# Kernel tuning notes

Measured on AMD Instinct MI355X. Metric: run time of the kernel, lower is better.

## Reference

```python
import jax, jax.numpy as jnp
import numpy as np

D_MODEL = 1024
NUM_HEADS = 16
HEAD_DIM = D_MODEL // NUM_HEADS
SEQ_LEN = 2048
BATCH = 2
THETA = 10000.0


def apply_rope(x, token_positions):
    # x: (..., seq, head_dim); token_positions: (seq,)
    d_k = x.shape[-1]
    inv_freq = 1.0 / (THETA ** (jnp.arange(0, d_k, 2, dtype=jnp.float32) / d_k))  # (d_k/2,)
    angle = token_positions.astype(jnp.float32)[:, None] * inv_freq[None, :]       # (seq, d_k/2)
    cos, sin = jnp.cos(angle), jnp.sin(angle)
    xr = x.reshape(*x.shape[:-1], d_k // 2, 2)
    a, b = xr[..., 0], xr[..., 1]  # real, imag parts of consecutive pairs
    # complex multiply (a + ib) * (cos + i sin)
    out_r = a * cos - b * sin
    out_i = a * sin + b * cos
    return jnp.stack([out_r, out_i], axis=-1).reshape(x.shape)


def setup_inputs() -> dict:
    key = jax.random.key(0)
    ks = jax.random.split(key, 5)
    std = np.sqrt(2.0 / (D_MODEL + D_MODEL))
    return {
        "x": jax.random.normal(ks[0], (BATCH, SEQ_LEN, D_MODEL), dtype=jnp.float32),
        "Wq": jax.random.normal(ks[1], (D_MODEL, D_MODEL), dtype=jnp.float32) * std,
        "Wk": jax.random.normal(ks[2], (D_MODEL, D_MODEL), dtype=jnp.float32) * std,
        "Wv": jax.random.normal(ks[3], (D_MODEL, D_MODEL), dtype=jnp.float32) * std,
        "Wo": jax.random.normal(ks[4], (D_MODEL, D_MODEL), dtype=jnp.float32) * std,
        "token_positions": jnp.arange(SEQ_LEN, dtype=jnp.int32),
    }


def reference(x, Wq, Wk, Wv, Wo, token_positions):
    B, L, D = x.shape
    H, Dh = NUM_HEADS, HEAD_DIM

    def proj(W):  # '... d_in, d_out d_in -> ... d_out' then split heads -> (B,H,L,Dh)
        y = jnp.einsum('bld,ed->ble', x, W)
        return y.reshape(B, L, H, Dh).transpose(0, 2, 1, 3)

    q = apply_rope(proj(Wq), token_positions)
    k = apply_rope(proj(Wk), token_positions)
    v = proj(Wv)

    scores = jnp.einsum('bhqd,bhkd->bhqk', q, k) / jnp.sqrt(jnp.float32(Dh))  # (B,H,L,L)
    causal = jnp.tril(jnp.ones((L, L), dtype=bool))
    scores = jnp.where(causal, scores, -jnp.inf)
    attn = jax.nn.softmax(scores, axis=-1)
    o = jnp.einsum('bhqk,bhkd->bhqd', attn, v)  # (B,H,L,Dh)
    o = o.transpose(0, 2, 1, 3).reshape(B, L, D)
    return jnp.einsum('bld,ed->ble', o, Wo)
```

## Files before the change

kernel.cpp:

```cpp
#include <hip/hip_runtime.h>

typedef __bf16 bf16;
typedef __attribute__((ext_vector_type(8))) __bf16 bf16x8;
typedef __attribute__((ext_vector_type(4))) __bf16 bf16x4;
typedef __attribute__((ext_vector_type(4))) float f32x4;

__device__ inline bf16 f2bf(float f) {
  unsigned u = __builtin_bit_cast(unsigned, f);
  u += 0x7fff + ((u >> 16) & 1);
  unsigned short h = (unsigned short)(u >> 16);
  return __builtin_bit_cast(bf16, h);
}

__device__ inline void gl_lds16(const bf16* g, bf16* l) {
  __builtin_amdgcn_global_load_lds(
      (const __attribute__((address_space(1))) void*)g,
      (__attribute__((address_space(3))) void*)l, 16, 0, 0);
}

__global__ __launch_bounds__(256) void cvt_kernel(
    const float* __restrict__ x, const float* __restrict__ wq,
    const float* __restrict__ wk, const float* __restrict__ wv,
    const float* __restrict__ wo, bf16* __restrict__ dst) {
  int idx = (blockIdx.x * 256 + threadIdx.x) * 4;
  const float* src;
  if (idx < 4194304) {
    src = x + idx;
  } else {
    int j = idx - 4194304;
    int w = j >> 20;
    const float* sw = (w == 0) ? wq : (w == 1) ? wk : (w == 2) ? wv : wo;
    src = sw + (j & 1048575);
  }
  float4 f = *(const float4*)src;
  bf16x4 o = {f2bf(f.x), f2bf(f.y), f2bf(f.z), f2bf(f.w)};
  *(bf16x4*)(dst + idx) = o;
}

__global__ __launch_bounds__(256) void rope_tab_kernel(
    const int* __restrict__ pos, float* __restrict__ tab) {
  int gid = blockIdx.x * 256 + threadIdx.x;
  int tok = gid >> 5, j = gid & 31;
  float freq = exp2f(-(float)(2 * j) * 0.20762051f);
  float angle = (float)pos[tok] * freq;
  float sn, cs;
  sincosf(angle, &sn, &cs);
  *(float2*)(tab + tok * 64 + j * 2) = make_float2(cs, sn);
}

__global__ __launch_bounds__(256) void gemm_qkv_kernel(
    const bf16* __restrict__ xb, const bf16* __restrict__ wb,
    const float* __restrict__ tab,
    bf16* __restrict__ Qb, bf16* __restrict__ Kb, bf16* __restrict__ Vtb) {
  __shared__ __align__(16) bf16 As[128 * 32];
  __shared__ __align__(16) bf16 Bs[128 * 32];
  int tid = threadIdx.x;
  int lane = tid & 63, w = tid >> 6;
  int l15 = lane & 15, quad = lane >> 4;
  int mb = blockIdx.y * 128, nb = blockIdx.x * 128;
  int mq = (w & 1) * 64, nq = (w >> 1) * 64;
  const bf16* agp = xb + (size_t)(mb + w * 16 + (lane >> 2)) * 1024 + (lane & 3) * 8;
  const bf16* bgp = wb + (size_t)(nb + w * 16 + (lane >> 2)) * 1024 + (lane & 3) * 8;
  bf16* alp = As + (w * 16) * 32;
  bf16* blp = Bs + (w * 16) * 32;
  f32x4 acc[4][4];
#pragma unroll
  for (int i = 0; i < 4; ++i)
#pragma unroll
    for (int j = 0; j < 4; ++j)
      for (int r = 0; r < 4; ++r) acc[i][j][r] = 0.f;
  for (int kt = 0; kt < 32; ++kt) {
    gl_lds16(agp, alp);
    gl_lds16(agp + 65536, alp + 2048);
    gl_lds16(bgp, blp);
    gl_lds16(bgp + 65536, blp + 2048);
    agp += 32; bgp += 32;
    __syncthreads();
    bf16x8 af[4], bfr[4];
#pragma unroll
    for (int mt = 0; mt < 4; ++mt)
      af[mt] = *(const bf16x8*)(As + (mq + mt * 16 + l15) * 32 + quad * 8);
#pragma unroll
    for (int nt = 0; nt < 4; ++nt)
      bfr[nt] = *(const bf16x8*)(Bs + (nq + nt * 16 + l15) * 32 + quad * 8);
#pragma unroll
    for (int mt = 0; mt < 4; ++mt)
#pragma unroll
      for (int nt = 0; nt < 4; ++nt)
        acc[mt][nt] = __builtin_amdgcn_mfma_f32_16x16x32_bf16(af[mt], bfr[nt], acc[mt][nt], 0, 0, 0);
    __syncthreads();
  }
#pragma unroll
  for (int nt = 0; nt < 4; ++nt) {
    int e = nb + nq + nt * 16 + l15;
    bool isv = (e >= 2048);
    int d = e & 63;
    int h = (e & 1023) >> 6;
    int tbase = d & ~1;
#pragma unroll
    for (int mt = 0; mt < 4; ++mt) {
#pragma unroll
      for (int r = 0; r < 4; ++r) {
        int m = mb + mq + mt * 16 + quad * 4 + r;
        int b = m >> 11, ltok = m & 2047;
        float val = acc[mt][nt][r];
        float p = __shfl_xor(val, 1);
        float outv;
        if (!isv) {
          float2 cs2 = *(const float2*)(tab + ltok * 64 + tbase);
          outv = (e & 1) ? (p * cs2.y + val * cs2.x) : (val * cs2.x - p * cs2.y);
        } else {
          outv = val;
        }
        bf16 bv = f2bf(outv);
        if (e < 1024) {
          Qb[(((b << 4) + h) * 2048 + ltok) * 64 + d] = bv;
        } else if (!isv) {
          Kb[(((b << 4) + h) * 2048 + ltok) * 64 + d] = bv;
        } else {
          Vtb[(((b << 4) + h) * 64 + d) * 2048 + ltok] = bv;
        }
      }
    }
  }
}

#define SCALE_L2E 0.18033688f
__global__ __launch_bounds__(256) void attn_kernel(
    const bf16* __restrict__ Qb, const bf16* __restrict__ Kb,
    const bf16* __restrict__ Vtb, bf16* __restrict__ Ob) {
  __shared__ __align__(16) bf16 Ks[64 * 64];
  __shared__ __align__(16) bf16 Vs[64 * 64];
  __shared__ __align__(16) bf16 pbuf[4][16 * 72];
  int tid = threadIdx.x;
  int lane = tid & 63, w = tid >> 6;
  int l15 = lane & 15, quad = lane >> 4;
  int bidx = blockIdx.x;
  int bh = bidx & 31;
  int qt = 31 - (bidx >> 5);
  int qbase = qt * 64;
  const bf16* Qp = Qb + (size_t)bh * 131072;
  const bf16* Kp = Kb + (size_t)bh * 131072;
  const bf16* Vp = Vtb + (size_t)bh * 131072;
  int r8 = lane >> 3;
  int gsw8 = (lane & 7) ^ r8;
  int g0 = quad ^ (l15 & 7);
  int g1 = (4 + quad) ^ (l15 & 7);
  bf16x8 qf[2];
#pragma unroll
  for (int c = 0; c < 2; ++c)
    qf[c] = *(const bf16x8*)(Qp + (size_t)(qbase + w * 16 + l15) * 64 + c * 32 + quad * 8);
  f32x4 oacc[4];
#pragma unroll
  for (int dt = 0; dt < 4; ++dt)
    for (int r = 0; r < 4; ++r) oacc[dt][r] = 0.f;
  float lpart = 0.f;
  int qmin_w = qbase + w * 16;
  int qmax_w = qmin_w + 15;
  int ntiles = qt + 1;

  for (int t = 0; t < ntiles; ++t) {
    int kb = t * 64;
    {
      const bf16* ksrc = Kp + (size_t)(kb + w * 16 + r8) * 64 + gsw8 * 8;
      bf16* kdst = &Ks[(w * 16) * 64];
      gl_lds16(ksrc, kdst);
      gl_lds16(ksrc + 8 * 64, kdst + 8 * 64);
      const bf16* vsrc = Vp + (size_t)(w * 16 + r8) * 2048 + kb + gsw8 * 8;
      bf16* vdst = &Vs[(w * 16) * 64];
      gl_lds16(vsrc, vdst);
      gl_lds16(vsrc + 8 * 2048, vdst + 8 * 64);
    }
    __syncthreads();
    if (kb <= qmax_w) {
      bf16x8 kf[4][2], vf[4][2];
#pragma unroll
      for (int kt = 0; kt < 4; ++kt) {
        kf[kt][0] = *(const bf16x8*)(&Ks[(kt * 16 + l15) * 64 + g0 * 8]);
        kf[kt][1] = *(const bf16x8*)(&Ks[(kt * 16 + l15) * 64 + g1 * 8]);
      }
#pragma unroll
      for (int dt = 0; dt < 4; ++dt) {
        vf[dt][0] = *(const bf16x8*)(&Vs[(dt * 16 + l15) * 64 + g0 * 8]);
        vf[dt][1] = *(const bf16x8*)(&Vs[(dt * 16 + l15) * 64 + g1 * 8]);
      }
      int q = qmin_w + l15;
      f32x4 s[4];
#pragma unroll
      for (int kt = 0; kt < 4; ++kt) {
        for (int r = 0; r < 4; ++r) s[kt][r] = 0.f;
        s[kt] = __builtin_amdgcn_mfma_f32_16x16x32_bf16(kf[kt][0], qf[0], s[kt], 0, 0, 0);
        s[kt] = __builtin_amdgcn_mfma_f32_16x16x32_bf16(kf[kt][1], qf[1], s[kt], 0, 0, 0);
      }
      float pe[16];
      if (kb + 63 > qmin_w) {
#pragma unroll
        for (int kt = 0; kt < 4; ++kt)
#pragma unroll
          for (int r = 0; r < 4; ++r) {
            int key = kb + kt * 16 + quad * 4 + r;
            pe[kt * 4 + r] = (key <= q) ? exp2f(s[kt][r] * SCALE_L2E) : 0.f;
          }
      } else {
#pragma unroll
        for (int kt = 0; kt < 4; ++kt)
#pragma unroll
          for (int r = 0; r < 4; ++r) pe[kt * 4 + r] = exp2f(s[kt][r] * SCALE_L2E);
      }
#pragma unroll
      for (int i = 0; i < 16; ++i) lpart += pe[i];
#pragma unroll
      for (int kt = 0; kt < 4; ++kt) {
        bf16x4 pw = {f2bf(pe[kt * 4]), f2bf(pe[kt * 4 + 1]), f2bf(pe[kt * 4 + 2]), f2bf(pe[kt * 4 + 3])};
        *(bf16x4*)&pbuf[w][l15 * 72 + kt * 16 + quad * 4] = pw;
      }
      bf16x8 pb0 = *(const bf16x8*)&pbuf[w][l15 * 72 + quad * 8];
      bf16x8 pb1 = *(const bf16x8*)&pbuf[w][l15 * 72 + 32 + quad * 8];
#pragma unroll
      for (int dt = 0; dt < 4; ++dt) {
        oacc[dt] = __builtin_amdgcn_mfma_f32_16x16x32_bf16(vf[dt][0], pb0, oacc[dt], 0, 0, 0);
        oacc[dt] = __builtin_amdgcn_mfma_f32_16x16x32_bf16(vf[dt][1], pb1, oacc[dt], 0, 0, 0);
      }
    }
    __syncthreads();
  }
  float lrun = lpart;
  lrun += __shfl_xor(lrun, 16);
  lrun += __shfl_xor(lrun, 32);
  int b0 = bh >> 4, h = bh & 15;
  float inv = 1.f / lrun;
  int q = qmin_w + l15;
  bf16* obase = Ob + ((size_t)(b0 * 2048 + q)) * 1024 + h * 64;
#pragma unroll
  for (int dt = 0; dt < 4; ++dt)
#pragma unroll
    for (int r = 0; r < 4; ++r)
      obase[dt * 16 + quad * 4 + r] = f2bf(oacc[dt][r] * inv);
}

__global__ __launch_bounds__(256) void gemm_out_kernel(
    const bf16* __restrict__ Ob, const bf16* __restrict__ wob,
    float* __restrict__ out) {
  __shared__ __align__(16) bf16 As[64 * 32];
  __shared__ __align__(16) bf16 Bs[64 * 32];
  int tid = threadIdx.x;
  int lane = tid & 63, w = tid >> 6;
  int l15 = lane & 15, quad = lane >> 4;
  int mb = blockIdx.y * 64, nb = blockIdx.x * 64;
  int mq = (w & 1) * 32, nq = (w >> 1) * 32;
  const bf16* agp = Ob + (size_t)(mb + w * 16 + (lane >> 2)) * 1024 + (lane & 3) * 8;
  const bf16* bgp = wob + (size_t)(nb + w * 16 + (lane >> 2)) * 1024 + (lane & 3) * 8;
  bf16* alp = As + (w * 16) * 32;
  bf16* blp = Bs + (w * 16) * 32;
  f32x4 acc[2][2];
#pragma unroll
  for (int i = 0; i < 2; ++i)
#pragma unroll
    for (int j = 0; j < 2; ++j)
      for (int r = 0; r < 4; ++r) acc[i][j][r] = 0.f;
  for (int kt = 0; kt < 32; ++kt) {
    gl_lds16(agp, alp);
    gl_lds16(bgp, blp);
    agp += 32; bgp += 32;
    __syncthreads();
    bf16x8 af[2], bfr[2];
#pragma unroll
    for (int mt = 0; mt < 2; ++mt)
      af[mt] = *(const bf16x8*)(As + (mq + mt * 16 + l15) * 32 + quad * 8);
#pragma unroll
    for (int nt = 0; nt < 2; ++nt)
      bfr[nt] = *(const bf16x8*)(Bs + (nq + nt * 16 + l15) * 32 + quad * 8);
#pragma unroll
    for (int mt = 0; mt < 2; ++mt)
#pragma unroll
      for (int nt = 0; nt < 2; ++nt)
        acc[mt][nt] = __builtin_amdgcn_mfma_f32_16x16x32_bf16(af[mt], bfr[nt], acc[mt][nt], 0, 0, 0);
    __syncthreads();
  }
#pragma unroll
  for (int mt = 0; mt < 2; ++mt)
#pragma unroll
    for (int nt = 0; nt < 2; ++nt)
#pragma unroll
      for (int r = 0; r < 4; ++r)
        out[(size_t)(mb + mq + mt * 16 + quad * 4 + r) * 1024 + nb + nq + nt * 16 + l15] = acc[mt][nt][r];
}

extern "C" void kernel_launch(void* const* d_in, const int* in_sizes, int n_in,
                              void* d_out, int out_size, void* d_ws, size_t ws_size,
                              hipStream_t stream) {
  const float* x  = (const float*)d_in[0];
  const float* wq = (const float*)d_in[1];
  const float* wk = (const float*)d_in[2];
  const float* wv = (const float*)d_in[3];
  const float* wo = (const float*)d_in[4];
  const int* pos  = (const int*)d_in[5];
  float* out = (float*)d_out;
  bf16* wsb = (bf16*)d_ws;
  bf16* xb  = wsb;
  bf16* wb  = wsb + 4194304;
  bf16* Qb  = wsb + 8388608;
  bf16* Kb  = wsb + 12582912;
  bf16* Vtb = wsb + 16777216;
  bf16* Obf = wsb + 20971520;
  float* tab = (float*)Obf;
  hipLaunchKernelGGL(cvt_kernel, dim3(8192), dim3(256), 0, stream, x, wq, wk, wv, wo, wsb);
  hipLaunchKernelGGL(rope_tab_kernel, dim3(256), dim3(256), 0, stream, pos, tab);
  hipLaunchKernelGGL(gemm_qkv_kernel, dim3(24, 32), dim3(256), 0, stream, xb, wb, tab, Qb, Kb, Vtb);
  hipLaunchKernelGGL(attn_kernel, dim3(1024), dim3(256), 0, stream, Qb, Kb, Vtb, Obf);
  hipLaunchKernelGGL(gemm_out_kernel, dim3(16, 64), dim3(256), 0, stream, Obf, wb + 3 * 1048576, out);
}
```

Measured before the change: 227.5 us.

## Restructure QKV GEMM with K=64 swizzled LDS tiles, block remap, and coalesced V stores

Merges the RoPE table computation into the conversion kernel to drop one launch. The QKV GEMM now loads K-tiles of 64 with an XOR-swizzled LDS layout to cut bank conflicts and halve the barrier count. It also remaps the 1D grid so neighbouring blocks share operands in cache. The V epilogue transposes through LDS so V^T is written with 16-byte coalesced stores instead of scattered 2-byte writes. In exchange it doubles LDS use per block and adds extra barriers in the V path.

```diff
diff --git a/kernel.cpp b/kernel.cpp
--- a/kernel.cpp
+++ b/kernel.cpp
@@ -21,7 +21,18 @@
 __global__ __launch_bounds__(256) void cvt_kernel(
     const float* __restrict__ x, const float* __restrict__ wq,
     const float* __restrict__ wk, const float* __restrict__ wv,
-    const float* __restrict__ wo, bf16* __restrict__ dst) {
+    const float* __restrict__ wo, bf16* __restrict__ dst,
+    const int* __restrict__ pos, float* __restrict__ tab) {
+  if (blockIdx.x >= 8192) {
+    int gid = (blockIdx.x - 8192) * 256 + threadIdx.x;
+    int tok = gid >> 5, j = gid & 31;
+    float freq = exp2f(-(float)(2 * j) * 0.20762051f);
+    float angle = (float)pos[tok] * freq;
+    float sn, cs;
+    sincosf(angle, &sn, &cs);
+    *(float2*)(tab + tok * 64 + j * 2) = make_float2(cs, sn);
+    return;
+  }
   int idx = (blockIdx.x * 256 + threadIdx.x) * 4;
   const float* src;
   if (idx < 4194304) {
@@ -37,90 +48,103 @@
   *(bf16x4*)(dst + idx) = o;
 }
 
-__global__ __launch_bounds__(256) void rope_tab_kernel(
-    const int* __restrict__ pos, float* __restrict__ tab) {
-  int gid = blockIdx.x * 256 + threadIdx.x;
-  int tok = gid >> 5, j = gid & 31;
-  float freq = exp2f(-(float)(2 * j) * 0.20762051f);
-  float angle = (float)pos[tok] * freq;
-  float sn, cs;
-  sincosf(angle, &sn, &cs);
-  *(float2*)(tab + tok * 64 + j * 2) = make_float2(cs, sn);
-}
-
 __global__ __launch_bounds__(256) void gemm_qkv_kernel(
     const bf16* __restrict__ xb, const bf16* __restrict__ wb,
     const float* __restrict__ tab,
     bf16* __restrict__ Qb, bf16* __restrict__ Kb, bf16* __restrict__ Vtb) {
-  __shared__ __align__(16) bf16 As[128 * 32];
-  __shared__ __align__(16) bf16 Bs[128 * 32];
+  __shared__ __align__(16) bf16 smem[16384];
+  bf16* As = smem;
+  bf16* Bs = smem + 8192;
   int tid = threadIdx.x;
   int lane = tid & 63, w = tid >> 6;
   int l15 = lane & 15, quad = lane >> 4;
-  int mb = blockIdx.y * 128, nb = blockIdx.x * 128;
+  int bid = blockIdx.x;
+  int sb = (bid & 7) * 96 + (bid >> 3);
+  int bx = sb % 24, by = sb / 24;
+  int mb = by * 128, nb = bx * 128;
   int mq = (w & 1) * 64, nq = (w >> 1) * 64;
-  const bf16* agp = xb + (size_t)(mb + w * 16 + (lane >> 2)) * 1024 + (lane & 3) * 8;
-  const bf16* bgp = wb + (size_t)(nb + w * 16 + (lane >> 2)) * 1024 + (lane & 3) * 8;
-  bf16* alp = As + (w * 16) * 32;
-  bf16* blp = Bs + (w * 16) * 32;
+  int gsw = (lane & 7) ^ ((lane >> 3) & 7);
+  const bf16* agp = xb + (size_t)(mb + w * 32 + (lane >> 3)) * 1024 + gsw * 8;
+  const bf16* bgp = wb + (size_t)(nb + w * 32 + (lane >> 3)) * 1024 + gsw * 8;
+  bf16* alp = As + (w * 32) * 64;
+  bf16* blp = Bs + (w * 32) * 64;
   f32x4 acc[4][4];
 #pragma unroll
   for (int i = 0; i < 4; ++i)
 #pragma unroll
     for (int j = 0; j < 4; ++j)
       for (int r = 0; r < 4; ++r) acc[i][j][r] = 0.f;
-  for (int kt = 0; kt < 32; ++kt) {
-    gl_lds16(agp, alp);
-    gl_lds16(agp + 65536, alp + 2048);
-    gl_lds16(bgp, blp);
-    gl_lds16(bgp + 65536, blp + 2048);
-    agp += 32; bgp += 32;
-    __syncthreads();
-    bf16x8 af[4], bfr[4];
-#pragma unroll
-    for (int mt = 0; mt < 4; ++mt)
-      af[mt] = *(const bf16x8*)(As + (mq + mt * 16 + l15) * 32 + quad * 8);
-#pragma unroll
-    for (int nt = 0; nt < 4; ++nt)
-      bfr[nt] = *(const bf16x8*)(Bs + (nq + nt * 16 + l15) * 32 + quad * 8);
-#pragma unroll
-    for (int mt = 0; mt < 4; ++mt)
+  for (int kt = 0; kt < 16; ++kt) {
+#pragma unroll
+    for (int i = 0; i < 4; ++i) {
+      gl_lds16(agp + i * 8192, alp + i * 512);
+      gl_lds16(bgp + i * 8192, blp + i * 512);
+    }
+    agp += 64; bgp += 64;
+    __syncthreads();
+#pragma unroll
+    for (int c = 0; c < 2; ++c) {
+      bf16x8 af[4], bfr[4];
+      int rg = (c * 4 + quad);
+#pragma unroll
+      for (int mt = 0; mt < 4; ++mt)
+        af[mt] = *(const bf16x8*)(As + (mq + mt * 16 + l15) * 64 + (rg ^ (l15 & 7)) * 8);
 #pragma unroll
       for (int nt = 0; nt < 4; ++nt)
-        acc[mt][nt] = __builtin_amdgcn_mfma_f32_16x16x32_bf16(af[mt], bfr[nt], acc[mt][nt], 0, 0, 0);
-    __syncthreads();
-  }
-#pragma unroll
-  for (int nt = 0; nt < 4; ++nt) {
-    int e = nb + nq + nt * 16 + l15;
-    bool isv = (e >= 2048);
-    int d = e & 63;
-    int h = (e & 1023) >> 6;
-    int tbase = d & ~1;
-#pragma unroll
-    for (int mt = 0; mt < 4; ++mt) {
-#pragma unroll
-      for (int r = 0; r < 4; ++r) {
-        int m = mb + mq + mt * 16 + quad * 4 + r;
-        int b = m >> 11, ltok = m & 2047;
-        float val = acc[mt][nt][r];
-        float p = __shfl_xor(val, 1);
-        float outv;
-        if (!isv) {
+        bfr[nt] = *(const bf16x8*)(Bs + (nq + nt * 16 + l15) * 64 + (rg ^ (l15 & 7)) * 8);
+#pragma unroll
+      for (int mt = 0; mt < 4; ++mt)
+#pragma unroll
+        for (int nt = 0; nt < 4; ++nt)
+          acc[mt][nt] = __builtin_amdgcn_mfma_f32_16x16x32_bf16(af[mt], bfr[nt], acc[mt][nt], 0, 0, 0);
+    }
+    __syncthreads();
+  }
+  int b = mb >> 11;
+  int mtok = mb & 2047;
+  if (bx < 16) {
+    bf16* dst = (bx < 8) ? Qb : Kb;
+#pragma unroll
+    for (int nt = 0; nt < 4; ++nt) {
+      int e = nb + nq + nt * 16 + l15;
+      int d = e & 63;
+      int h = (e & 1023) >> 6;
+      int tbase = d & ~1;
+#pragma unroll
+      for (int mt = 0; mt < 4; ++mt) {
+#pragma unroll
+        for (int r = 0; r < 4; ++r) {
+          int ltok = mtok + mq + mt * 16 + quad * 4 + r;
+          float val = acc[mt][nt][r];
+          float p = __shfl_xor(val, 1);
           float2 cs2 = *(const float2*)(tab + ltok * 64 + tbase);
-          outv = (e & 1) ? (p * cs2.y + val * cs2.x) : (val * cs2.x - p * cs2.y);
-        } else {
-          outv = val;
+          float outv = (e & 1) ? (p * cs2.y + val * cs2.x) : (val * cs2.x - p * cs2.y);
+          dst[(size_t)(((b << 4) + h) * 2048 + ltok) * 64 + d] = f2bf(outv);
         }
-        bf16 bv = f2bf(outv);
-        if (e < 1024) {
-          Qb[(((b << 4) + h) * 2048 + ltok) * 64 + d] = bv;
-        } else if (!isv) {
-          Kb[(((b << 4) + h) * 2048 + ltok) * 64 + d] = bv;
-        } else {
-          Vtb[(((b << 4) + h) * 64 + d) * 2048 + ltok] = bv;
-        }
-      }
+      }
+    }
+  } else {
+    bf16* T = smem;
+    for (int h2 = 0; h2 < 2; ++h2) {
+      if ((w >> 1) == h2) {
+#pragma unroll
+        for (int nt = 0; nt < 4; ++nt)
+#pragma unroll
+          for (int mt = 0; mt < 4; ++mt) {
+            bf16x4 tv = {f2bf(acc[mt][nt][0]), f2bf(acc[mt][nt][1]),
+                         f2bf(acc[mt][nt][2]), f2bf(acc[mt][nt][3])};
+            *(bf16x4*)&T[(nt * 16 + l15) * 136 + mq + mt * 16 + quad * 4] = tv;
+          }
+      }
+      __syncthreads();
+      int row = tid >> 2, cs = (tid & 3) * 32;
+      int e = nb + h2 * 64 + row;
+      int d = e & 63, hh = (e & 1023) >> 6;
+      bf16* vdst = Vtb + ((size_t)((b << 4) + hh) * 64 + d) * 2048 + mtok + cs;
+#pragma unroll
+      for (int j = 0; j < 4; ++j)
+        *(bf16x8*)(vdst + j * 8) = *(const bf16x8*)&T[row * 136 + cs + j * 8];
+      __syncthreads();
     }
   }
 }
@@ -304,9 +328,8 @@
   bf16* Vtb = wsb + 16777216;
   bf16* Obf = wsb + 20971520;
   float* tab = (float*)Obf;
-  hipLaunchKernelGGL(cvt_kernel, dim3(8192), dim3(256), 0, stream, x, wq, wk, wv, wo, wsb);
-  hipLaunchKernelGGL(rope_tab_kernel, dim3(256), dim3(256), 0, stream, pos, tab);
-  hipLaunchKernelGGL(gemm_qkv_kernel, dim3(24, 32), dim3(256), 0, stream, xb, wb, tab, Qb, Kb, Vtb);
+  hipLaunchKernelGGL(cvt_kernel, dim3(8448), dim3(256), 0, stream, x, wq, wk, wv, wo, wsb, pos, tab);
+  hipLaunchKernelGGL(gemm_qkv_kernel, dim3(768), dim3(256), 0, stream, xb, wb, tab, Qb, Kb, Vtb);
   hipLaunchKernelGGL(attn_kernel, dim3(1024), dim3(256), 0, stream, Qb, Kb, Vtb, Obf);
   hipLaunchKernelGGL(gemm_out_kernel, dim3(16, 64), dim3(256), 0, stream, Obf, wb + 3 * 1048576, out);
 }
```

Measured after the change: 203.3 us. 1.12x faster.
